# Performance work log

Measured on AMD Instinct MI355X. Metric: run time of the kernel, lower is better.

The kernel has to match this reference:

```python
import jax, jax.numpy as jnp
import numpy as np

B, N = 16, 300000          # batch, total anchors per image (all FPN levels concatenated)
PRE, POST = 2000, 1000     # num_pre_nms, num_post_nms
NMS_THR = 0.7
MIN_SIZE = 1e-3            # proposal_min_size
IMG_H, IMG_W = 800.0, 1333.0


def setup_inputs() -> dict:
    key = jax.random.key(0)
    k1, k2, k3, k4, k5, k6 = jax.random.split(key, 6)
    cls = jax.random.normal(k1, (B, N), dtype=jnp.float32)
    reg = jax.random.normal(k2, (B, N, 4), dtype=jnp.float32) * 0.1
    # anchors as valid (cx,cy,w,h)->(x1,y1,x2,y2) boxes inside the image
    cx = jax.random.uniform(k3, (B, N), dtype=jnp.float32, minval=0.0, maxval=IMG_W)
    cy = jax.random.uniform(k4, (B, N), dtype=jnp.float32, minval=0.0, maxval=IMG_H)
    w = jax.random.uniform(k5, (B, N), dtype=jnp.float32, minval=16.0, maxval=256.0)
    h = jax.random.uniform(k6, (B, N), dtype=jnp.float32, minval=16.0, maxval=256.0)
    anchors = jnp.stack([cx - 0.5 * w, cy - 0.5 * h, cx + 0.5 * w, cy + 0.5 * h], axis=-1)
    return {"cls": cls, "reg": reg, "anchors": anchors}


def _decode(anchor, reg):
    aw = anchor[:, 2] - anchor[:, 0]
    ah = anchor[:, 3] - anchor[:, 1]
    acx = anchor[:, 0] + 0.5 * aw
    acy = anchor[:, 1] + 0.5 * ah
    dx, dy, dw, dh = reg[:, 0], reg[:, 1], reg[:, 2], reg[:, 3]
    pcx = dx * aw + acx
    pcy = dy * ah + acy
    pw = jnp.exp(dw) * aw
    ph = jnp.exp(dh) * ah
    return jnp.stack([pcx - 0.5 * pw, pcy - 0.5 * ph, pcx + 0.5 * pw, pcy + 0.5 * ph], axis=-1)


def _iou_matrix(boxes):
    # boxes: [K,4] -> pairwise IoU [K,K]
    area = (boxes[:, 2] - boxes[:, 0]) * (boxes[:, 3] - boxes[:, 1])
    lt = jnp.maximum(boxes[:, None, :2], boxes[None, :, :2])
    rb = jnp.minimum(boxes[:, None, 2:], boxes[None, :, 2:])
    wh = jnp.clip(rb - lt, 0.0)
    inter = wh[..., 0] * wh[..., 1]
    union = area[:, None] + area[None, :] - inter
    return inter / jnp.maximum(union, 1e-8)


def _per_image(score, reg, anchor):
    # topk pre-NMS selection (lax.top_k returns score-descending order)
    top_s, idx = jax.lax.top_k(score, PRE)
    boxes = _decode(anchor[idx], reg[idx].reshape(-1, 4))
    # clip to image bounds
    bounds = jnp.array([IMG_W, IMG_H, IMG_W, IMG_H], dtype=boxes.dtype)
    boxes = jnp.clip(boxes, 0.0, bounds)
    # remove small boxes (mask instead of dynamic removal)
    w = boxes[:, 2] - boxes[:, 0]
    h = boxes[:, 3] - boxes[:, 1]
    valid = (w >= MIN_SIZE) & (h >= MIN_SIZE)
    s = jnp.where(valid, top_s, -jnp.inf)
    order = jnp.argsort(-s)  # score-descending, invalid last
    boxes = boxes[order]
    valid = valid[order]
    # greedy NMS: iterate highest-score-first, suppress later boxes with IoU > thr
    iou = _iou_matrix(boxes)
    rng = jnp.arange(PRE)
    def body(i, keep):
        sup = (iou[i] > NMS_THR) & keep[i]
        return keep & jnp.logical_not(sup & (rng > i))
    keep = jax.lax.fori_loop(0, PRE, body, valid)
    # gather kept boxes (score order preserved), pad with zeros past count
    sel = jnp.argsort(jnp.logical_not(keep), stable=True)[:POST]
    return boxes[sel] * keep[sel][:, None].astype(boxes.dtype)


def reference(cls, reg, anchors):
    # [B, POST, 4] proposals per image (zero-padded where fewer than POST kept)
    return jax.vmap(_per_image)(cls, reg, anchors)
```

## Files before the change

kernel.cpp:

```cpp
#include <hip/hip_runtime.h>

#define NB 16
#define NN 300000
#define PRE 2000
#define POST 1000

typedef unsigned long long ull;

static const size_t OFF_HIST1   = 0;
static const size_t OFF_CANDCNT = 65536;
static const size_t OFF_BINCNT  = 65792;
static const size_t OFF_B1      = 66048;
static const size_t OFF_NEED1   = 66304;
static const size_t OFF_NVALID  = 66560;
static const size_t OFF_BITMAP  = 66816;
static const size_t ZERO_BYTES  = 70912;
static const size_t OFF_CAND    = 70912;
static const size_t OFF_KEYS    = 201984;
static const size_t OFF_BOXTMP  = 464128;
static const size_t OFF_SORTED  = 988416;
static const size_t OFF_MASK    = 1500416;
static const size_t OFF_BINBUF  = OFF_MASK;

__device__ __forceinline__ unsigned f2u(float f){
  unsigned b = __float_as_uint(f);
  return (b & 0x80000000u) ? ~b : (b | 0x80000000u);
}

#define H1REP 8
#define H1STRIDE 1025
__global__ void k_hist1(const float* __restrict__ cls, unsigned* __restrict__ hist){
  __shared__ unsigned h[H1REP * H1STRIDE];
  int img = blockIdx.y;
  for (int i = threadIdx.x; i < H1REP * H1STRIDE; i += blockDim.x) h[i] = 0;
  __syncthreads();
  const float* p = cls + (size_t)img * NN;
  int stride = gridDim.x * blockDim.x;
  unsigned rep = (threadIdx.x & (H1REP - 1)) * H1STRIDE;
  for (int i = blockIdx.x * blockDim.x + threadIdx.x; i < NN; i += stride)
    atomicAdd(&h[rep + (f2u(p[i]) >> 22)], 1u);
  __syncthreads();
  unsigned* g = hist + img * 1024;
  for (int i = threadIdx.x; i < 1024; i += blockDim.x){
    unsigned v = 0;
    for (int r = 0; r < H1REP; r++) v += h[r * H1STRIDE + i];
    if (v) atomicAdd(&g[i], v);
  }
}

__global__ void k_scan(const unsigned* __restrict__ hist, int bins,
                       unsigned K0,
                       unsigned* __restrict__ outBin, unsigned* __restrict__ outNeed){
  int img = blockIdx.x;
  int t = threadIdx.x;
  const unsigned* hh = hist + img * bins;
  unsigned K = K0;
  int per = bins >> 8;
  unsigned s = 0;
  for (int q = 0; q < per; q++) s += hh[bins - 1 - (t * per + q)];
  __shared__ unsigned arr[256];
  arr[t] = s;
  __syncthreads();
  for (int off = 1; off < 256; off <<= 1){
    unsigned v = (t >= off) ? arr[t - off] : 0u;
    __syncthreads();
    arr[t] += v;
    __syncthreads();
  }
  unsigned incl = arr[t], excl = incl - s;
  if (excl < K && K <= incl){
    unsigned c = excl;
    for (int q = 0; q < per; q++){
      int b = bins - 1 - (t * per + q);
      unsigned cnt = hh[b];
      if (c + cnt >= K){ outBin[img] = (unsigned)b; outNeed[img] = K - c; break; }
      c += cnt;
    }
  }
}

__global__ void k_compactA(const float* __restrict__ cls, const unsigned* __restrict__ b1,
                           unsigned* __restrict__ cand, unsigned* __restrict__ candCnt,
                           ull* __restrict__ binbuf, unsigned* __restrict__ binCnt){
  __shared__ unsigned lc[1024];
  __shared__ ull lb[512];
  __shared__ unsigned lcn, lbn, baseC, baseB;
  int img = blockIdx.y;
  if (threadIdx.x == 0){ lcn = 0; lbn = 0; }
  __syncthreads();
  unsigned bb1 = b1[img];
  const float* p = cls + (size_t)img * NN;
  int stride = gridDim.x * blockDim.x;
  for (int i = blockIdx.x * blockDim.x + threadIdx.x; i < NN; i += stride){
    unsigned u = f2u(p[i]);
    unsigned top = u >> 22;
    if (top > bb1){
      unsigned pos = atomicAdd(&lcn, 1u);
      if (pos < 1024u) lc[pos] = (unsigned)i;
      else { unsigned g = atomicAdd(&candCnt[img], 1u); if (g < 2048u) cand[img * 2048 + g] = (unsigned)i; }
    } else if (top == bb1){
      ull e = ((ull)u << 32) | (unsigned)i;
      unsigned pos = atomicAdd(&lbn, 1u);
      if (pos < 512u) lb[pos] = e;
      else { unsigned g = atomicAdd(&binCnt[img], 1u); if (g < 8192u) binbuf[img * 8192 + g] = e; }
    }
  }
  __syncthreads();
  unsigned nc = lcn < 1024u ? lcn : 1024u;
  unsigned nb = lbn < 512u ? lbn : 512u;
  if (threadIdx.x == 0){
    if (nc) baseC = atomicAdd(&candCnt[img], nc);
    if (nb) baseB = atomicAdd(&binCnt[img], nb);
  }
  __syncthreads();
  for (unsigned t = threadIdx.x; t < nc; t += blockDim.x){
    unsigned g = baseC + t;
    if (g < 2048u) cand[img * 2048 + g] = lc[t];
  }
  for (unsigned t = threadIdx.x; t < nb; t += blockDim.x){
    unsigned g = baseB + t;
    if (g < 8192u) binbuf[img * 8192 + g] = lb[t];
  }
}

__global__ __launch_bounds__(256) void k_select(const float* __restrict__ cls,
                                                const float* __restrict__ reg,
                                                const float* __restrict__ anch,
                                                unsigned* __restrict__ cand,
                                                const unsigned* __restrict__ candCnt,
                                                const ull* __restrict__ binbuf,
                                                const unsigned* __restrict__ binCnt,
                                                const unsigned* __restrict__ need1,
                                                float* __restrict__ boxTmp,
                                                ull* __restrict__ keys,
                                                unsigned* __restrict__ nvalid){
  __shared__ unsigned hist[2048];
  __shared__ unsigned arr[256];
  __shared__ unsigned b2s, need2s, b3s, need3s;
  __shared__ unsigned tiePos[1024];
  __shared__ unsigned wcnt, tieCnt;
  int img = blockIdx.x, tid = threadIdx.x;
  unsigned bc = binCnt[img]; if (bc > 8192u) bc = 8192u;
  unsigned base = candCnt[img];
  unsigned need = need1[img];
  const ull* bb = binbuf + img * 8192;

  if (tid == 0){ wcnt = 0; tieCnt = 0; b2s = 0; need2s = 0; b3s = 0; need3s = 0; }
  for (int i = tid; i < 2048; i += 256) hist[i] = 0;
  __syncthreads();
  for (unsigned t = tid; t < bc; t += 256){
    unsigned u = (unsigned)(bb[t] >> 32);
    atomicAdd(&hist[(u >> 11) & 0x7FFu], 1u);
  }
  __syncthreads();
  {
    unsigned s = 0;
    for (int q = 0; q < 8; q++) s += hist[2047 - (tid * 8 + q)];
    arr[tid] = s; __syncthreads();
    for (int off = 1; off < 256; off <<= 1){
      unsigned v = (tid >= off) ? arr[tid - off] : 0u;
      __syncthreads(); arr[tid] += v; __syncthreads();
    }
    unsigned incl = arr[tid], excl = incl - s;
    if (excl < need && need <= incl){
      unsigned c = excl;
      for (int q = 0; q < 8; q++){
        int b = 2047 - (tid * 8 + q);
        unsigned cnt = hist[b];
        if (c + cnt >= need){ b2s = (unsigned)b; need2s = need - c; break; }
        c += cnt;
      }
    }
  }
  __syncthreads();
  unsigned b2 = b2s, need2 = need2s;
  for (int i = tid; i < 2048; i += 256) hist[i] = 0;
  __syncthreads();
  for (unsigned t = tid; t < bc; t += 256){
    unsigned u = (unsigned)(bb[t] >> 32);
    if (((u >> 11) & 0x7FFu) == b2) atomicAdd(&hist[u & 0x7FFu], 1u);
  }
  __syncthreads();
  {
    unsigned s = 0;
    for (int q = 0; q < 8; q++) s += hist[2047 - (tid * 8 + q)];
    arr[tid] = s; __syncthreads();
    for (int off = 1; off < 256; off <<= 1){
      unsigned v = (tid >= off) ? arr[tid - off] : 0u;
      __syncthreads(); arr[tid] += v; __syncthreads();
    }
    unsigned incl = arr[tid], excl = incl - s;
    if (excl < need2 && need2 <= incl){
      unsigned c = excl;
      for (int q = 0; q < 8; q++){
        int b = 2047 - (tid * 8 + q);
        unsigned cnt = hist[b];
        if (c + cnt >= need2){ b3s = (unsigned)b; need3s = need2 - c; break; }
        c += cnt;
      }
    }
  }
  __syncthreads();
  unsigned b3 = b3s, need3 = need3s;
  for (unsigned t = tid; t < bc; t += 256){
    ull e = bb[t];
    unsigned u = (unsigned)(e >> 32);
    unsigned mid = (u >> 11) & 0x7FFu, low = u & 0x7FFu;
    bool take = (mid > b2) || (mid == b2 && low > b3);
    bool tie  = (mid == b2) && (low == b3);
    if (take){
      unsigned p = atomicAdd(&wcnt, 1u);
      unsigned g = base + p;
      if (g < 2048u) cand[img * 2048 + g] = (unsigned)(e & 0xFFFFFFFFull);
    } else if (tie){
      unsigned p = atomicAdd(&tieCnt, 1u);
      if (p < 1024u) tiePos[p] = t;
    }
  }
  __syncthreads();
  unsigned above = wcnt;
  unsigned ec = tieCnt; if (ec > 1024u) ec = 1024u;
  for (unsigned t = tid; t < ec; t += 256){
    unsigned idx = (unsigned)(bb[tiePos[t]] & 0xFFFFFFFFull);
    unsigned r = 0;
    for (unsigned s = 0; s < ec; s++){
      unsigned idx2 = (unsigned)(bb[tiePos[s]] & 0xFFFFFFFFull);
      r += (idx2 < idx) ? 1u : 0u;
    }
    if (r < need3){
      unsigned g = base + above + r;
      if (g < 2048u) cand[img * 2048 + g] = idx;
    }
  }
  __syncthreads();
  for (int slot = tid; slot < 2048; slot += 256){
    ull key = 0ull;
    float4 box = make_float4(0.f, 0.f, 0.f, 0.f);
    bool counted = false;
    if (slot < PRE){
      unsigned i = cand[img * 2048 + slot];
      if (i < NN){
        size_t gi = (size_t)img * NN + i;
        float4 a = ((const float4*)anch)[gi];
        float4 r = ((const float4*)reg)[gi];
        float sc = cls[gi];
        float aw = a.z - a.x, ah = a.w - a.y;
        float acx = a.x + 0.5f * aw, acy = a.y + 0.5f * ah;
        float pcx = r.x * aw + acx, pcy = r.y * ah + acy;
        float pw = expf(r.z) * aw, ph = expf(r.w) * ah;
        float x1 = pcx - 0.5f * pw, y1 = pcy - 0.5f * ph;
        float x2 = pcx + 0.5f * pw, y2 = pcy + 0.5f * ph;
        x1 = fminf(fmaxf(x1, 0.f), 1333.f); x2 = fminf(fmaxf(x2, 0.f), 1333.f);
        y1 = fminf(fmaxf(y1, 0.f), 800.f);  y2 = fminf(fmaxf(y2, 0.f), 800.f);
        bool valid = ((x2 - x1) >= 0.001f) && ((y2 - y1) >= 0.001f);
        unsigned up = valid ? f2u(sc) : 0u;
        key = ((ull)up << 32) | (ull)(0xFFFFFFFFu - i);
        box = make_float4(x1, y1, x2, y2);
        counted = valid;
      }
    }
    keys[img * 2048 + slot] = key;
    ((float4*)boxTmp)[img * 2048 + slot] = box;
    ull bal = __ballot(counted);
    if ((tid & 63) == 0 && bal)
      atomicAdd(&nvalid[img], (unsigned)__popcll(bal));
  }
}

__global__ __launch_bounds__(256) void k_rank(const ull* __restrict__ keys,
                                              const float* __restrict__ boxTmp,
                                              float* __restrict__ sorted){
  __shared__ ull lk[2048];
  int img = blockIdx.y;
  int e = blockIdx.x * 256 + threadIdx.x;
  for (int t = threadIdx.x; t < 2048; t += 256) lk[t] = keys[img * 2048 + t];
  __syncthreads();
  ull me = lk[e];
  unsigned rank = 0;
  #pragma unroll 8
  for (int j = 0; j < 2048; j++) rank += (lk[j] > me) ? 1u : 0u;
  if (rank < PRE)
    ((float4*)sorted)[img * PRE + rank] = ((const float4*)boxTmp)[img * 2048 + e];
}

__global__ __launch_bounds__(512) void k_mask(const float* __restrict__ sorted,
                                              const unsigned* __restrict__ nvalid,
                                              ull* __restrict__ mask, ull* __restrict__ bitmap){
  __shared__ float4 bx[PRE];
  __shared__ float  ar[PRE];
  int img = blockIdx.y, tid = threadIdx.x;
  int jmin = blockIdx.x * 16;
  for (int i = jmin + tid; i < PRE; i += 512){
    float4 b = ((const float4*)sorted)[img * PRE + i];
    bx[i] = b;
    ar[i] = (b.z - b.x) * (b.w - b.y);
  }
  __syncthreads();
  int unit = tid >> 5;
  int w = tid & 31;
  int lane = tid & 63;
  int nv = (int)nvalid[img];
  int qhi = ((PRE - 1 - w) >> 5) + 1;
  int rowF = jmin + unit;
  #pragma unroll
  for (int rr = 0; rr < 2; rr++){
    int row = (rr == 0) ? rowF : (PRE - 1 - rowF);
    float4 bi = bx[row];
    float ai = ar[row];
    int qlo = (row >= w) ? (((row - w) >> 5) + 1) : 0;
    ull m = 0;
    for (int q = qlo; q < qhi; q++){
      int j = (q << 5) + w;
      float4 bj = bx[j];
      float xx1 = fmaxf(bi.x, bj.x), yy1 = fmaxf(bi.y, bj.y);
      float xx2 = fminf(bi.z, bj.z), yy2 = fminf(bi.w, bj.w);
      float ww = fmaxf(xx2 - xx1, 0.f), hh = fmaxf(yy2 - yy1, 0.f);
      float inter = ww * hh;
      float uni = ai + ar[j] - inter;
      if (inter / fmaxf(uni, 1e-8f) > 0.7f) m |= (1ull << q);
    }
    mask[((size_t)(img * PRE + row)) * 32 + w] = m;
    ull nz = __ballot(m != 0ull);
    if (lane == 0 || lane == 32){
      ull half = (lane == 0) ? (nz & 0xFFFFFFFFull) : (nz >> 32);
      if (half && row < nv)
        atomicOr(&bitmap[img * 32 + (row >> 6)], 1ull << (row & 63));
    }
  }
}

#define CHR 48
__global__ __launch_bounds__(256) void k_nms(const ull* __restrict__ mask,
                                             const ull* __restrict__ bitmap,
                                             const unsigned* __restrict__ nvalid,
                                             const float* __restrict__ sorted,
                                             float* __restrict__ out){
  __shared__ unsigned rowsLds[2048];
  __shared__ unsigned cntw[32];
  __shared__ unsigned wbaseS[32];
  __shared__ int mcountS, mpS;
  __shared__ ull cacheD[2][CHR * 32];
  __shared__ ull keepP[32];
  __shared__ ull keepLin[32];
  __shared__ unsigned cntArr[32], preArr[32];
  int img = blockIdx.x, tid = threadIdx.x;
  int lane = tid & 63, wave = tid >> 6;

  if (tid < 32) cntw[tid] = (unsigned)__popcll(bitmap[img * 32 + tid]);
  __syncthreads();
  if (tid == 0){
    unsigned s = 0;
    for (int w0 = 0; w0 < 32; w0++){ wbaseS[w0] = s; s += cntw[w0]; }
    mcountS = (int)s;
    mpS = ((int)s + CHR - 1) / CHR * CHR;
  }
  __syncthreads();
  int m = mcountS, mp = mpS;
  if (tid < 32){
    ull bits = bitmap[img * 32 + tid];
    unsigned pos = wbaseS[tid];
    int base_i = tid * 64;
    while (bits){
      int b = __ffsll((long long)bits) - 1;
      rowsLds[pos++] = (unsigned)(base_i + b);
      bits &= bits - 1;
    }
  }
  for (int t = m + tid; t < mp; t += 256) rowsLds[t] = PRE - 1;
  __syncthreads();

  int nch = mp / CHR;
  ull remv = 0;
  const ull* mg = mask + (size_t)img * PRE * 32;

  if (nch > 0 && tid >= 64){
    int s = tid - 64;
    ull v[8];
    #pragma unroll
    for (int k = 0; k < 8; k++){
      int t = k * 192 + s;
      unsigned rr = rowsLds[t >> 5];
      v[k] = mg[(size_t)rr * 32 + (t & 31)];
    }
    #pragma unroll
    for (int k = 0; k < 8; k++) cacheD[0][k * 192 + s] = v[k];
  }
  __syncthreads();

  for (int c = 0; c < nch; c++){
    int cb = c & 1;
    if (tid >= 64){
      if (c + 1 < nch){
        int q0n = (c + 1) * CHR;
        int s = tid - 64;
        ull v[8];
        #pragma unroll
        for (int k = 0; k < 8; k++){
          int t = k * 192 + s;
          unsigned rr = rowsLds[q0n + (t >> 5)];
          v[k] = mg[(size_t)rr * 32 + (t & 31)];
        }
        #pragma unroll
        for (int k = 0; k < 8; k++) cacheD[cb ^ 1][k * 192 + s] = v[k];
      }
    } else {
      const ull* cbuf = cacheD[cb];
      const int q0 = c * CHR;
      ull cur[8]; unsigned ci[8];
      #pragma unroll
      for (int k = 0; k < 8; k++){
        ci[k] = rowsLds[q0 + k];
        cur[k] = cbuf[(k << 5) | (lane & 31)];
      }
      #pragma unroll
      for (int g = 0; g < 6; g++){
        ull nxt[8]; unsigned ni[8];
        if (g < 5){
          #pragma unroll
          for (int k = 0; k < 8; k++){
            int lq = (g + 1) * 8 + k;
            ni[k] = rowsLds[q0 + lq];
            nxt[k] = cbuf[(lq << 5) | (lane & 31)];
          }
        }
        #pragma unroll
        for (int k = 0; k < 8; k++){
          unsigned i = ci[k];
          unsigned bit = ((unsigned)(remv >> (i >> 5))) & 1u;
          int sup = (lane == (int)(i & 31)) && bit;
          if (!__any(sup)) remv |= cur[k];
        }
        if (g < 5){
          #pragma unroll
          for (int k = 0; k < 8; k++){ cur[k] = nxt[k]; ci[k] = ni[k]; }
        }
      }
    }
    __syncthreads();
  }

  int nv = (int)nvalid[img];
  if (wave == 0 && lane < 32){
    int cnt2 = (nv > lane) ? (((nv - 1 - lane) >> 5) + 1) : 0;
    ull vm = (cnt2 >= 64) ? ~0ull : ((1ull << cnt2) - 1ull);
    keepP[lane] = (~remv) & vm;
  }
  __syncthreads();
  if (tid < 32){
    ull lin = 0;
    for (int kk = 0; kk < 64; kk++)
      lin |= ((keepP[kk & 31] >> (2 * tid + (kk >> 5))) & 1ull) << kk;
    keepLin[tid] = lin;
    cntArr[tid] = (unsigned)__popcll(lin);
  }
  __syncthreads();
  if (tid < 32){
    unsigned pre = 0;
    for (int w0 = 0; w0 < tid; w0++) pre += cntArr[w0];
    preArr[tid] = pre;
  }
  __syncthreads();
  int totK = (int)(preArr[31] + cntArr[31]);
  for (int i = tid; i < PRE; i += 256){
    int w0 = i >> 6, b = i & 63;
    ull kw = keepLin[w0];
    if ((kw >> b) & 1ull){
      unsigned rank = preArr[w0] + (unsigned)__popcll(kw & ((1ull << b) - 1ull));
      if (rank < POST)
        ((float4*)out)[img * POST + rank] = ((const float4*)sorted)[img * PRE + i];
    }
  }
  for (int r = totK + tid; r < POST; r += 256)
    ((float4*)out)[img * POST + r] = make_float4(0.f, 0.f, 0.f, 0.f);
}

extern "C" void kernel_launch(void* const* d_in, const int* in_sizes, int n_in,
                              void* d_out, int out_size, void* d_ws, size_t ws_size,
                              hipStream_t stream){
  const float* cls  = (const float*)d_in[0];
  const float* reg  = (const float*)d_in[1];
  const float* anch = (const float*)d_in[2];
  float* out = (float*)d_out;
  char* ws = (char*)d_ws;

  unsigned* hist1   = (unsigned*)(ws + OFF_HIST1);
  unsigned* candCnt = (unsigned*)(ws + OFF_CANDCNT);
  unsigned* binCnt  = (unsigned*)(ws + OFF_BINCNT);
  unsigned* b1      = (unsigned*)(ws + OFF_B1);
  unsigned* need1   = (unsigned*)(ws + OFF_NEED1);
  unsigned* nvalid  = (unsigned*)(ws + OFF_NVALID);
  ull*      bitmap  = (ull*)     (ws + OFF_BITMAP);
  unsigned* cand    = (unsigned*)(ws + OFF_CAND);
  ull*      keys    = (ull*)     (ws + OFF_KEYS);
  float*    boxTmp  = (float*)   (ws + OFF_BOXTMP);
  float*    sorted  = (float*)   (ws + OFF_SORTED);
  ull*      maskG   = (ull*)     (ws + OFF_MASK);
  ull*      binbuf  = (ull*)     (ws + OFF_BINBUF);

  hipMemsetAsync(ws, 0, ZERO_BYTES, stream);

  k_hist1   <<<dim3(64, NB), 256, 0, stream>>>(cls, hist1);
  k_scan    <<<NB, 256, 0, stream>>>(hist1, 1024, 2000u, b1, need1);
  k_compactA<<<dim3(64, NB), 256, 0, stream>>>(cls, b1, cand, candCnt, binbuf, binCnt);
  k_select  <<<NB, 256, 0, stream>>>(cls, reg, anch, cand, candCnt, binbuf, binCnt,
                                     need1, boxTmp, keys, nvalid);
  k_rank    <<<dim3(8, NB), 256, 0, stream>>>(keys, boxTmp, sorted);
  k_mask    <<<dim3(63, NB), 512, 0, stream>>>(sorted, nvalid, maskG, bitmap);
  k_nms     <<<NB, 256, 0, stream>>>(maskG, bitmap, nvalid, sorted, out);
}
```

Measured before the change: 302.5 us.

## Fuse score histogram with speculative high-score stash; drop scan and compaction kernels

The histogram kernel now also appends (key, index) pairs for every score whose top 10 bits are at or above a fixed bin into a per-image stash. The threshold scan and the second full compaction pass over the scores are removed; k_select computes the first threshold itself and filters candidates from the stash. If the chosen bin falls below the stash threshold, or the stash overflows, it falls back to scanning all scores. This removes one full read of the score array and two kernel launches. In exchange it adds stash writes in the histogram pass and longer single-block loops in k_select, and it adds an unroll hint to the IoU mask loop.

```diff
diff --git a/kernel.cpp b/kernel.cpp
--- a/kernel.cpp
+++ b/kernel.cpp
@@ -8,10 +8,7 @@
 typedef unsigned long long ull;
 
 static const size_t OFF_HIST1   = 0;
-static const size_t OFF_CANDCNT = 65536;
-static const size_t OFF_BINCNT  = 65792;
-static const size_t OFF_B1      = 66048;
-static const size_t OFF_NEED1   = 66304;
+static const size_t OFF_STASHC  = 65536;
 static const size_t OFF_NVALID  = 66560;
 static const size_t OFF_BITMAP  = 66816;
 static const size_t ZERO_BYTES  = 70912;
@@ -20,7 +17,10 @@
 static const size_t OFF_BOXTMP  = 464128;
 static const size_t OFF_SORTED  = 988416;
 static const size_t OFF_MASK    = 1500416;
-static const size_t OFF_BINBUF  = OFF_MASK;
+static const size_t OFF_STASH   = OFF_MASK;
+
+#define BSTAT 767u
+#define STCAP 32768u
 
 __device__ __forceinline__ unsigned f2u(float f){
   unsigned b = __float_as_uint(f);
@@ -29,17 +29,37 @@
 
 #define H1REP 8
 #define H1STRIDE 1025
-__global__ void k_hist1(const float* __restrict__ cls, unsigned* __restrict__ hist){
+__global__ void k_histstash(const float* __restrict__ cls, unsigned* __restrict__ hist,
+                            ull* __restrict__ stash, unsigned* __restrict__ stashCnt){
   __shared__ unsigned h[H1REP * H1STRIDE];
+  __shared__ ull lb[512];
+  __shared__ unsigned lbn, baseB;
   int img = blockIdx.y;
   for (int i = threadIdx.x; i < H1REP * H1STRIDE; i += blockDim.x) h[i] = 0;
+  if (threadIdx.x == 0) lbn = 0;
   __syncthreads();
   const float* p = cls + (size_t)img * NN;
   int stride = gridDim.x * blockDim.x;
   unsigned rep = (threadIdx.x & (H1REP - 1)) * H1STRIDE;
-  for (int i = blockIdx.x * blockDim.x + threadIdx.x; i < NN; i += stride)
-    atomicAdd(&h[rep + (f2u(p[i]) >> 22)], 1u);
-  __syncthreads();
+  ull* st = stash + (size_t)img * STCAP;
+  for (int i = blockIdx.x * blockDim.x + threadIdx.x; i < NN; i += stride){
+    unsigned u = f2u(p[i]);
+    atomicAdd(&h[rep + (u >> 22)], 1u);
+    if ((u >> 22) >= BSTAT){
+      ull e = ((ull)u << 32) | (unsigned)i;
+      unsigned pos = atomicAdd(&lbn, 1u);
+      if (pos < 512u) lb[pos] = e;
+      else { unsigned g = atomicAdd(&stashCnt[img], 1u); if (g < STCAP) st[g] = e; }
+    }
+  }
+  __syncthreads();
+  unsigned nb = lbn < 512u ? lbn : 512u;
+  if (threadIdx.x == 0 && nb) baseB = atomicAdd(&stashCnt[img], nb);
+  __syncthreads();
+  for (unsigned t = threadIdx.x; t < nb; t += blockDim.x){
+    unsigned g = baseB + t;
+    if (g < STCAP) st[g] = lb[t];
+  }
   unsigned* g = hist + img * 1024;
   for (int i = threadIdx.x; i < 1024; i += blockDim.x){
     unsigned v = 0;
@@ -48,109 +68,64 @@
   }
 }
 
-__global__ void k_scan(const unsigned* __restrict__ hist, int bins,
-                       unsigned K0,
-                       unsigned* __restrict__ outBin, unsigned* __restrict__ outNeed){
-  int img = blockIdx.x;
-  int t = threadIdx.x;
-  const unsigned* hh = hist + img * bins;
-  unsigned K = K0;
-  int per = bins >> 8;
-  unsigned s = 0;
-  for (int q = 0; q < per; q++) s += hh[bins - 1 - (t * per + q)];
-  __shared__ unsigned arr[256];
-  arr[t] = s;
-  __syncthreads();
-  for (int off = 1; off < 256; off <<= 1){
-    unsigned v = (t >= off) ? arr[t - off] : 0u;
-    __syncthreads();
-    arr[t] += v;
-    __syncthreads();
-  }
-  unsigned incl = arr[t], excl = incl - s;
-  if (excl < K && K <= incl){
-    unsigned c = excl;
-    for (int q = 0; q < per; q++){
-      int b = bins - 1 - (t * per + q);
-      unsigned cnt = hh[b];
-      if (c + cnt >= K){ outBin[img] = (unsigned)b; outNeed[img] = K - c; break; }
-      c += cnt;
-    }
-  }
-}
-
-__global__ void k_compactA(const float* __restrict__ cls, const unsigned* __restrict__ b1,
-                           unsigned* __restrict__ cand, unsigned* __restrict__ candCnt,
-                           ull* __restrict__ binbuf, unsigned* __restrict__ binCnt){
-  __shared__ unsigned lc[1024];
-  __shared__ ull lb[512];
-  __shared__ unsigned lcn, lbn, baseC, baseB;
-  int img = blockIdx.y;
-  if (threadIdx.x == 0){ lcn = 0; lbn = 0; }
-  __syncthreads();
-  unsigned bb1 = b1[img];
-  const float* p = cls + (size_t)img * NN;
-  int stride = gridDim.x * blockDim.x;
-  for (int i = blockIdx.x * blockDim.x + threadIdx.x; i < NN; i += stride){
-    unsigned u = f2u(p[i]);
-    unsigned top = u >> 22;
-    if (top > bb1){
-      unsigned pos = atomicAdd(&lcn, 1u);
-      if (pos < 1024u) lc[pos] = (unsigned)i;
-      else { unsigned g = atomicAdd(&candCnt[img], 1u); if (g < 2048u) cand[img * 2048 + g] = (unsigned)i; }
-    } else if (top == bb1){
-      ull e = ((ull)u << 32) | (unsigned)i;
-      unsigned pos = atomicAdd(&lbn, 1u);
-      if (pos < 512u) lb[pos] = e;
-      else { unsigned g = atomicAdd(&binCnt[img], 1u); if (g < 8192u) binbuf[img * 8192 + g] = e; }
-    }
-  }
-  __syncthreads();
-  unsigned nc = lcn < 1024u ? lcn : 1024u;
-  unsigned nb = lbn < 512u ? lbn : 512u;
-  if (threadIdx.x == 0){
-    if (nc) baseC = atomicAdd(&candCnt[img], nc);
-    if (nb) baseB = atomicAdd(&binCnt[img], nb);
-  }
-  __syncthreads();
-  for (unsigned t = threadIdx.x; t < nc; t += blockDim.x){
-    unsigned g = baseC + t;
-    if (g < 2048u) cand[img * 2048 + g] = lc[t];
-  }
-  for (unsigned t = threadIdx.x; t < nb; t += blockDim.x){
-    unsigned g = baseB + t;
-    if (g < 8192u) binbuf[img * 8192 + g] = lb[t];
-  }
-}
-
 __global__ __launch_bounds__(256) void k_select(const float* __restrict__ cls,
                                                 const float* __restrict__ reg,
                                                 const float* __restrict__ anch,
+                                                const unsigned* __restrict__ hist1,
                                                 unsigned* __restrict__ cand,
-                                                const unsigned* __restrict__ candCnt,
-                                                const ull* __restrict__ binbuf,
-                                                const unsigned* __restrict__ binCnt,
-                                                const unsigned* __restrict__ need1,
+                                                const ull* __restrict__ stash,
+                                                const unsigned* __restrict__ stashCnt,
                                                 float* __restrict__ boxTmp,
                                                 ull* __restrict__ keys,
                                                 unsigned* __restrict__ nvalid){
   __shared__ unsigned hist[2048];
   __shared__ unsigned arr[256];
-  __shared__ unsigned b2s, need2s, b3s, need3s;
+  __shared__ unsigned b1s, need1s, b2s, need2s, b3s, need3s;
   __shared__ unsigned tiePos[1024];
   __shared__ unsigned wcnt, tieCnt;
   int img = blockIdx.x, tid = threadIdx.x;
-  unsigned bc = binCnt[img]; if (bc > 8192u) bc = 8192u;
-  unsigned base = candCnt[img];
-  unsigned need = need1[img];
-  const ull* bb = binbuf + img * 8192;
-
-  if (tid == 0){ wcnt = 0; tieCnt = 0; b2s = 0; need2s = 0; b3s = 0; need3s = 0; }
+  const float* pcls = cls + (size_t)img * NN;
+  const ull* st = stash + (size_t)img * STCAP;
+
+  if (tid == 0){ wcnt = 0; tieCnt = 0; b1s = 0; need1s = 0; b2s = 0; need2s = 0; b3s = 0; need3s = 0; }
+  {
+    const unsigned* hh = hist1 + img * 1024;
+    unsigned s = 0;
+    for (int q = 0; q < 4; q++) s += hh[1023 - (tid * 4 + q)];
+    arr[tid] = s; __syncthreads();
+    for (int off = 1; off < 256; off <<= 1){
+      unsigned v = (tid >= off) ? arr[tid - off] : 0u;
+      __syncthreads(); arr[tid] += v; __syncthreads();
+    }
+    unsigned incl = arr[tid], excl = incl - s;
+    if (excl < 2000u && 2000u <= incl){
+      unsigned c = excl;
+      for (int q = 0; q < 4; q++){
+        int b = 1023 - (tid * 4 + q);
+        unsigned cnt = hh[b];
+        if (c + cnt >= 2000u){ b1s = (unsigned)b; need1s = 2000u - c; break; }
+        c += cnt;
+      }
+    }
+  }
   for (int i = tid; i < 2048; i += 256) hist[i] = 0;
   __syncthreads();
-  for (unsigned t = tid; t < bc; t += 256){
-    unsigned u = (unsigned)(bb[t] >> 32);
-    atomicAdd(&hist[(u >> 11) & 0x7FFu], 1u);
+  unsigned b1 = b1s, need = need1s;
+  unsigned sc = stashCnt[img];
+  bool fb = (b1 < BSTAT) || (sc > STCAP);
+  unsigned Nit = fb ? (unsigned)NN : sc;
+
+  for (unsigned t = tid; t < Nit; t += 256){
+    unsigned u, idx;
+    if (fb){ u = f2u(pcls[t]); idx = t; }
+    else { ull e = st[t]; u = (unsigned)(e >> 32); idx = (unsigned)(e & 0xFFFFFFFFull); }
+    unsigned top = u >> 22;
+    if (top > b1){
+      unsigned p = atomicAdd(&wcnt, 1u);
+      if (p < 2048u) cand[img * 2048 + p] = idx;
+    } else if (top == b1){
+      atomicAdd(&hist[(u >> 11) & 0x7FFu], 1u);
+    }
   }
   __syncthreads();
   {
@@ -176,9 +151,11 @@
   unsigned b2 = b2s, need2 = need2s;
   for (int i = tid; i < 2048; i += 256) hist[i] = 0;
   __syncthreads();
-  for (unsigned t = tid; t < bc; t += 256){
-    unsigned u = (unsigned)(bb[t] >> 32);
-    if (((u >> 11) & 0x7FFu) == b2) atomicAdd(&hist[u & 0x7FFu], 1u);
+  for (unsigned t = tid; t < Nit; t += 256){
+    unsigned u;
+    if (fb) u = f2u(pcls[t]);
+    else u = (unsigned)(st[t] >> 32);
+    if ((u >> 22) == b1 && ((u >> 11) & 0x7FFu) == b2) atomicAdd(&hist[u & 0x7FFu], 1u);
   }
   __syncthreads();
   {
@@ -202,33 +179,34 @@
   }
   __syncthreads();
   unsigned b3 = b3s, need3 = need3s;
-  for (unsigned t = tid; t < bc; t += 256){
-    ull e = bb[t];
-    unsigned u = (unsigned)(e >> 32);
+  for (unsigned t = tid; t < Nit; t += 256){
+    unsigned u, idx;
+    if (fb){ u = f2u(pcls[t]); idx = t; }
+    else { ull e = st[t]; u = (unsigned)(e >> 32); idx = (unsigned)(e & 0xFFFFFFFFull); }
+    if ((u >> 22) != b1) continue;
     unsigned mid = (u >> 11) & 0x7FFu, low = u & 0x7FFu;
     bool take = (mid > b2) || (mid == b2 && low > b3);
     bool tie  = (mid == b2) && (low == b3);
     if (take){
       unsigned p = atomicAdd(&wcnt, 1u);
-      unsigned g = base + p;
-      if (g < 2048u) cand[img * 2048 + g] = (unsigned)(e & 0xFFFFFFFFull);
+      if (p < 2048u) cand[img * 2048 + p] = idx;
     } else if (tie){
       unsigned p = atomicAdd(&tieCnt, 1u);
       if (p < 1024u) tiePos[p] = t;
     }
   }
   __syncthreads();
-  unsigned above = wcnt;
+  unsigned tbase = wcnt;
   unsigned ec = tieCnt; if (ec > 1024u) ec = 1024u;
   for (unsigned t = tid; t < ec; t += 256){
-    unsigned idx = (unsigned)(bb[tiePos[t]] & 0xFFFFFFFFull);
+    unsigned idx = fb ? tiePos[t] : (unsigned)(st[tiePos[t]] & 0xFFFFFFFFull);
     unsigned r = 0;
     for (unsigned s = 0; s < ec; s++){
-      unsigned idx2 = (unsigned)(bb[tiePos[s]] & 0xFFFFFFFFull);
+      unsigned idx2 = fb ? tiePos[s] : (unsigned)(st[tiePos[s]] & 0xFFFFFFFFull);
       r += (idx2 < idx) ? 1u : 0u;
     }
     if (r < need3){
-      unsigned g = base + above + r;
+      unsigned g = tbase + r;
       if (g < 2048u) cand[img * 2048 + g] = idx;
     }
   }
@@ -243,7 +221,7 @@
         size_t gi = (size_t)img * NN + i;
         float4 a = ((const float4*)anch)[gi];
         float4 r = ((const float4*)reg)[gi];
-        float sc = cls[gi];
+        float sc2 = cls[gi];
         float aw = a.z - a.x, ah = a.w - a.y;
         float acx = a.x + 0.5f * aw, acy = a.y + 0.5f * ah;
         float pcx = r.x * aw + acx, pcy = r.y * ah + acy;
@@ -253,7 +231,7 @@
         x1 = fminf(fmaxf(x1, 0.f), 1333.f); x2 = fminf(fmaxf(x2, 0.f), 1333.f);
         y1 = fminf(fmaxf(y1, 0.f), 800.f);  y2 = fminf(fmaxf(y2, 0.f), 800.f);
         bool valid = ((x2 - x1) >= 0.001f) && ((y2 - y1) >= 0.001f);
-        unsigned up = valid ? f2u(sc) : 0u;
+        unsigned up = valid ? f2u(sc2) : 0u;
         key = ((ull)up << 32) | (ull)(0xFFFFFFFFu - i);
         box = make_float4(x1, y1, x2, y2);
         counted = valid;
@@ -309,6 +287,7 @@
     float ai = ar[row];
     int qlo = (row >= w) ? (((row - w) >> 5) + 1) : 0;
     ull m = 0;
+    #pragma unroll 2
     for (int q = qlo; q < qhi; q++){
       int j = (q << 5) + w;
       float4 bj = bx[j];
@@ -483,28 +462,23 @@
   float* out = (float*)d_out;
   char* ws = (char*)d_ws;
 
-  unsigned* hist1   = (unsigned*)(ws + OFF_HIST1);
-  unsigned* candCnt = (unsigned*)(ws + OFF_CANDCNT);
-  unsigned* binCnt  = (unsigned*)(ws + OFF_BINCNT);
-  unsigned* b1      = (unsigned*)(ws + OFF_B1);
-  unsigned* need1   = (unsigned*)(ws + OFF_NEED1);
-  unsigned* nvalid  = (unsigned*)(ws + OFF_NVALID);
-  ull*      bitmap  = (ull*)     (ws + OFF_BITMAP);
-  unsigned* cand    = (unsigned*)(ws + OFF_CAND);
-  ull*      keys    = (ull*)     (ws + OFF_KEYS);
-  float*    boxTmp  = (float*)   (ws + OFF_BOXTMP);
-  float*    sorted  = (float*)   (ws + OFF_SORTED);
-  ull*      maskG   = (ull*)     (ws + OFF_MASK);
-  ull*      binbuf  = (ull*)     (ws + OFF_BINBUF);
+  unsigned* hist1    = (unsigned*)(ws + OFF_HIST1);
+  unsigned* stashCnt = (unsigned*)(ws + OFF_STASHC);
+  unsigned* nvalid   = (unsigned*)(ws + OFF_NVALID);
+  ull*      bitmap   = (ull*)     (ws + OFF_BITMAP);
+  unsigned* cand     = (unsigned*)(ws + OFF_CAND);
+  ull*      keys     = (ull*)     (ws + OFF_KEYS);
+  float*    boxTmp   = (float*)   (ws + OFF_BOXTMP);
+  float*    sorted   = (float*)   (ws + OFF_SORTED);
+  ull*      maskG    = (ull*)     (ws + OFF_MASK);
+  ull*      stash    = (ull*)     (ws + OFF_STASH);
 
   hipMemsetAsync(ws, 0, ZERO_BYTES, stream);
 
-  k_hist1   <<<dim3(64, NB), 256, 0, stream>>>(cls, hist1);
-  k_scan    <<<NB, 256, 0, stream>>>(hist1, 1024, 2000u, b1, need1);
-  k_compactA<<<dim3(64, NB), 256, 0, stream>>>(cls, b1, cand, candCnt, binbuf, binCnt);
-  k_select  <<<NB, 256, 0, stream>>>(cls, reg, anch, cand, candCnt, binbuf, binCnt,
-                                     need1, boxTmp, keys, nvalid);
-  k_rank    <<<dim3(8, NB), 256, 0, stream>>>(keys, boxTmp, sorted);
-  k_mask    <<<dim3(63, NB), 512, 0, stream>>>(sorted, nvalid, maskG, bitmap);
-  k_nms     <<<NB, 256, 0, stream>>>(maskG, bitmap, nvalid, sorted, out);
-}
+  k_histstash<<<dim3(64, NB), 256, 0, stream>>>(cls, hist1, stash, stashCnt);
+  k_select   <<<NB, 256, 0, stream>>>(cls, reg, anch, hist1, cand, stash, stashCnt,
+                                      boxTmp, keys, nvalid);
+  k_rank     <<<dim3(8, NB), 256, 0, stream>>>(keys, boxTmp, sorted);
+  k_mask     <<<dim3(63, NB), 512, 0, stream>>>(sorted, nvalid, maskG, bitmap);
+  k_nms      <<<NB, 256, 0, stream>>>(maskG, bitmap, nvalid, sorted, out);
+}
```

After: 343.9 us. +13.7%, slower.

## Stash high-score candidates during histogram pass to skip second full scan

Applied to the files above, without the earlier changes.

The histogram kernel now also writes every element whose top bits are at or above a fixed threshold bin into a per-image stash buffer. The compaction kernel then scans only this small stash instead of re-reading all 300k scores, with a fallback to the full scan when the selection bin falls below the threshold or the stash overflows. This removes the second full pass over the score array and lets compaction run with fewer blocks. In exchange the histogram pass does extra atomics and global writes, and it needs more workspace. The IoU mask loop also gets an unroll pragma.

```diff
diff --git a/kernel.cpp b/kernel.cpp
--- a/kernel.cpp
+++ b/kernel.cpp
@@ -8,19 +8,24 @@
 typedef unsigned long long ull;
 
 static const size_t OFF_HIST1   = 0;
-static const size_t OFF_CANDCNT = 65536;
-static const size_t OFF_BINCNT  = 65792;
-static const size_t OFF_B1      = 66048;
-static const size_t OFF_NEED1   = 66304;
-static const size_t OFF_NVALID  = 66560;
-static const size_t OFF_BITMAP  = 66816;
-static const size_t ZERO_BYTES  = 70912;
-static const size_t OFF_CAND    = 70912;
-static const size_t OFF_KEYS    = 201984;
-static const size_t OFF_BOXTMP  = 464128;
-static const size_t OFF_SORTED  = 988416;
-static const size_t OFF_MASK    = 1500416;
-static const size_t OFF_BINBUF  = OFF_MASK;
+static const size_t OFF_STASHC  = 65536;
+static const size_t OFF_CANDCNT = 65792;
+static const size_t OFF_BINCNT  = 66048;
+static const size_t OFF_B1      = 66304;
+static const size_t OFF_NEED1   = 66560;
+static const size_t OFF_NVALID  = 66816;
+static const size_t OFF_BITMAP  = 67072;
+static const size_t ZERO_BYTES  = 71168;
+static const size_t OFF_CAND    = 71168;
+static const size_t OFF_KEYS    = 202240;
+static const size_t OFF_BOXTMP  = 464384;
+static const size_t OFF_SORTED  = 988672;
+static const size_t OFF_MASK    = 1500672;
+static const size_t OFF_STASH   = OFF_MASK;
+static const size_t OFF_BINBUF  = OFF_MASK + 4194304;
+
+#define BSTAT 767u
+#define STCAP 32768u
 
 __device__ __forceinline__ unsigned f2u(float f){
   unsigned b = __float_as_uint(f);
@@ -29,17 +34,37 @@
 
 #define H1REP 8
 #define H1STRIDE 1025
-__global__ void k_hist1(const float* __restrict__ cls, unsigned* __restrict__ hist){
+__global__ void k_histstash(const float* __restrict__ cls, unsigned* __restrict__ hist,
+                            ull* __restrict__ stash, unsigned* __restrict__ stashCnt){
   __shared__ unsigned h[H1REP * H1STRIDE];
+  __shared__ ull lb[512];
+  __shared__ unsigned lbn, baseB;
   int img = blockIdx.y;
   for (int i = threadIdx.x; i < H1REP * H1STRIDE; i += blockDim.x) h[i] = 0;
+  if (threadIdx.x == 0) lbn = 0;
   __syncthreads();
   const float* p = cls + (size_t)img * NN;
   int stride = gridDim.x * blockDim.x;
   unsigned rep = (threadIdx.x & (H1REP - 1)) * H1STRIDE;
-  for (int i = blockIdx.x * blockDim.x + threadIdx.x; i < NN; i += stride)
-    atomicAdd(&h[rep + (f2u(p[i]) >> 22)], 1u);
-  __syncthreads();
+  ull* st = stash + (size_t)img * STCAP;
+  for (int i = blockIdx.x * blockDim.x + threadIdx.x; i < NN; i += stride){
+    unsigned u = f2u(p[i]);
+    atomicAdd(&h[rep + (u >> 22)], 1u);
+    if ((u >> 22) >= BSTAT){
+      ull e = ((ull)u << 32) | (unsigned)i;
+      unsigned pos = atomicAdd(&lbn, 1u);
+      if (pos < 512u) lb[pos] = e;
+      else { unsigned g = atomicAdd(&stashCnt[img], 1u); if (g < STCAP) st[g] = e; }
+    }
+  }
+  __syncthreads();
+  unsigned nb = lbn < 512u ? lbn : 512u;
+  if (threadIdx.x == 0 && nb) baseB = atomicAdd(&stashCnt[img], nb);
+  __syncthreads();
+  for (unsigned t = threadIdx.x; t < nb; t += blockDim.x){
+    unsigned g = baseB + t;
+    if (g < STCAP) st[g] = lb[t];
+  }
   unsigned* g = hist + img * 1024;
   for (int i = threadIdx.x; i < 1024; i += blockDim.x){
     unsigned v = 0;
@@ -48,16 +73,14 @@
   }
 }
 
-__global__ void k_scan(const unsigned* __restrict__ hist, int bins,
-                       unsigned K0,
+__global__ void k_scan(const unsigned* __restrict__ hist, unsigned K0,
                        unsigned* __restrict__ outBin, unsigned* __restrict__ outNeed){
   int img = blockIdx.x;
   int t = threadIdx.x;
-  const unsigned* hh = hist + img * bins;
+  const unsigned* hh = hist + img * 1024;
   unsigned K = K0;
-  int per = bins >> 8;
   unsigned s = 0;
-  for (int q = 0; q < per; q++) s += hh[bins - 1 - (t * per + q)];
+  for (int q = 0; q < 4; q++) s += hh[1023 - (t * 4 + q)];
   __shared__ unsigned arr[256];
   arr[t] = s;
   __syncthreads();
@@ -70,8 +93,8 @@
   unsigned incl = arr[t], excl = incl - s;
   if (excl < K && K <= incl){
     unsigned c = excl;
-    for (int q = 0; q < per; q++){
-      int b = bins - 1 - (t * per + q);
+    for (int q = 0; q < 4; q++){
+      int b = 1023 - (t * 4 + q);
       unsigned cnt = hh[b];
       if (c + cnt >= K){ outBin[img] = (unsigned)b; outNeed[img] = K - c; break; }
       c += cnt;
@@ -79,7 +102,8 @@
   }
 }
 
-__global__ void k_compactA(const float* __restrict__ cls, const unsigned* __restrict__ b1,
+__global__ void k_compactS(const float* __restrict__ cls, const ull* __restrict__ stash,
+                           const unsigned* __restrict__ stashCnt, const unsigned* __restrict__ b1,
                            unsigned* __restrict__ cand, unsigned* __restrict__ candCnt,
                            ull* __restrict__ binbuf, unsigned* __restrict__ binCnt){
   __shared__ unsigned lc[1024];
@@ -89,20 +113,39 @@
   if (threadIdx.x == 0){ lcn = 0; lbn = 0; }
   __syncthreads();
   unsigned bb1 = b1[img];
-  const float* p = cls + (size_t)img * NN;
+  unsigned sc = stashCnt[img];
+  bool fb = (bb1 < BSTAT) || (sc > STCAP);
   int stride = gridDim.x * blockDim.x;
-  for (int i = blockIdx.x * blockDim.x + threadIdx.x; i < NN; i += stride){
-    unsigned u = f2u(p[i]);
-    unsigned top = u >> 22;
-    if (top > bb1){
-      unsigned pos = atomicAdd(&lcn, 1u);
-      if (pos < 1024u) lc[pos] = (unsigned)i;
-      else { unsigned g = atomicAdd(&candCnt[img], 1u); if (g < 2048u) cand[img * 2048 + g] = (unsigned)i; }
-    } else if (top == bb1){
-      ull e = ((ull)u << 32) | (unsigned)i;
-      unsigned pos = atomicAdd(&lbn, 1u);
-      if (pos < 512u) lb[pos] = e;
-      else { unsigned g = atomicAdd(&binCnt[img], 1u); if (g < 8192u) binbuf[img * 8192 + g] = e; }
+  if (!fb){
+    const ull* st = stash + (size_t)img * STCAP;
+    for (unsigned t = blockIdx.x * blockDim.x + threadIdx.x; t < sc; t += (unsigned)stride){
+      ull e = st[t];
+      unsigned top = (unsigned)(e >> 54);
+      if (top > bb1){
+        unsigned pos = atomicAdd(&lcn, 1u);
+        if (pos < 1024u) lc[pos] = (unsigned)(e & 0xFFFFFFFFull);
+        else { unsigned g = atomicAdd(&candCnt[img], 1u); if (g < 2048u) cand[img * 2048 + g] = (unsigned)(e & 0xFFFFFFFFull); }
+      } else if (top == bb1){
+        unsigned pos = atomicAdd(&lbn, 1u);
+        if (pos < 512u) lb[pos] = e;
+        else { unsigned g = atomicAdd(&binCnt[img], 1u); if (g < 8192u) binbuf[img * 8192 + g] = e; }
+      }
+    }
+  } else {
+    const float* p = cls + (size_t)img * NN;
+    for (int i = blockIdx.x * blockDim.x + threadIdx.x; i < NN; i += stride){
+      unsigned u = f2u(p[i]);
+      unsigned top = u >> 22;
+      if (top > bb1){
+        unsigned pos = atomicAdd(&lcn, 1u);
+        if (pos < 1024u) lc[pos] = (unsigned)i;
+        else { unsigned g = atomicAdd(&candCnt[img], 1u); if (g < 2048u) cand[img * 2048 + g] = (unsigned)i; }
+      } else if (top == bb1){
+        ull e = ((ull)u << 32) | (unsigned)i;
+        unsigned pos = atomicAdd(&lbn, 1u);
+        if (pos < 512u) lb[pos] = e;
+        else { unsigned g = atomicAdd(&binCnt[img], 1u); if (g < 8192u) binbuf[img * 8192 + g] = e; }
+      }
     }
   }
   __syncthreads();
@@ -243,7 +286,7 @@
         size_t gi = (size_t)img * NN + i;
         float4 a = ((const float4*)anch)[gi];
         float4 r = ((const float4*)reg)[gi];
-        float sc = cls[gi];
+        float sc2 = cls[gi];
         float aw = a.z - a.x, ah = a.w - a.y;
         float acx = a.x + 0.5f * aw, acy = a.y + 0.5f * ah;
         float pcx = r.x * aw + acx, pcy = r.y * ah + acy;
@@ -253,7 +296,7 @@
         x1 = fminf(fmaxf(x1, 0.f), 1333.f); x2 = fminf(fmaxf(x2, 0.f), 1333.f);
         y1 = fminf(fmaxf(y1, 0.f), 800.f);  y2 = fminf(fmaxf(y2, 0.f), 800.f);
         bool valid = ((x2 - x1) >= 0.001f) && ((y2 - y1) >= 0.001f);
-        unsigned up = valid ? f2u(sc) : 0u;
+        unsigned up = valid ? f2u(sc2) : 0u;
         key = ((ull)up << 32) | (ull)(0xFFFFFFFFu - i);
         box = make_float4(x1, y1, x2, y2);
         counted = valid;
@@ -309,6 +352,7 @@
     float ai = ar[row];
     int qlo = (row >= w) ? (((row - w) >> 5) + 1) : 0;
     ull m = 0;
+    #pragma unroll 2
     for (int q = qlo; q < qhi; q++){
       int j = (q << 5) + w;
       float4 bj = bx[j];
@@ -483,28 +527,30 @@
   float* out = (float*)d_out;
   char* ws = (char*)d_ws;
 
-  unsigned* hist1   = (unsigned*)(ws + OFF_HIST1);
-  unsigned* candCnt = (unsigned*)(ws + OFF_CANDCNT);
-  unsigned* binCnt  = (unsigned*)(ws + OFF_BINCNT);
-  unsigned* b1      = (unsigned*)(ws + OFF_B1);
-  unsigned* need1   = (unsigned*)(ws + OFF_NEED1);
-  unsigned* nvalid  = (unsigned*)(ws + OFF_NVALID);
-  ull*      bitmap  = (ull*)     (ws + OFF_BITMAP);
-  unsigned* cand    = (unsigned*)(ws + OFF_CAND);
-  ull*      keys    = (ull*)     (ws + OFF_KEYS);
-  float*    boxTmp  = (float*)   (ws + OFF_BOXTMP);
-  float*    sorted  = (float*)   (ws + OFF_SORTED);
-  ull*      maskG   = (ull*)     (ws + OFF_MASK);
-  ull*      binbuf  = (ull*)     (ws + OFF_BINBUF);
+  unsigned* hist1    = (unsigned*)(ws + OFF_HIST1);
+  unsigned* stashCnt = (unsigned*)(ws + OFF_STASHC);
+  unsigned* candCnt  = (unsigned*)(ws + OFF_CANDCNT);
+  unsigned* binCnt   = (unsigned*)(ws + OFF_BINCNT);
+  unsigned* b1       = (unsigned*)(ws + OFF_B1);
+  unsigned* need1    = (unsigned*)(ws + OFF_NEED1);
+  unsigned* nvalid   = (unsigned*)(ws + OFF_NVALID);
+  ull*      bitmap   = (ull*)     (ws + OFF_BITMAP);
+  unsigned* cand     = (unsigned*)(ws + OFF_CAND);
+  ull*      keys     = (ull*)     (ws + OFF_KEYS);
+  float*    boxTmp   = (float*)   (ws + OFF_BOXTMP);
+  float*    sorted   = (float*)   (ws + OFF_SORTED);
+  ull*      maskG    = (ull*)     (ws + OFF_MASK);
+  ull*      stash    = (ull*)     (ws + OFF_STASH);
+  ull*      binbuf   = (ull*)     (ws + OFF_BINBUF);
 
   hipMemsetAsync(ws, 0, ZERO_BYTES, stream);
 
-  k_hist1   <<<dim3(64, NB), 256, 0, stream>>>(cls, hist1);
-  k_scan    <<<NB, 256, 0, stream>>>(hist1, 1024, 2000u, b1, need1);
-  k_compactA<<<dim3(64, NB), 256, 0, stream>>>(cls, b1, cand, candCnt, binbuf, binCnt);
-  k_select  <<<NB, 256, 0, stream>>>(cls, reg, anch, cand, candCnt, binbuf, binCnt,
-                                     need1, boxTmp, keys, nvalid);
-  k_rank    <<<dim3(8, NB), 256, 0, stream>>>(keys, boxTmp, sorted);
-  k_mask    <<<dim3(63, NB), 512, 0, stream>>>(sorted, nvalid, maskG, bitmap);
-  k_nms     <<<NB, 256, 0, stream>>>(maskG, bitmap, nvalid, sorted, out);
-}
+  k_histstash<<<dim3(64, NB), 256, 0, stream>>>(cls, hist1, stash, stashCnt);
+  k_scan     <<<NB, 256, 0, stream>>>(hist1, 2000u, b1, need1);
+  k_compactS <<<dim3(8, NB), 256, 0, stream>>>(cls, stash, stashCnt, b1, cand, candCnt, binbuf, binCnt);
+  k_select   <<<NB, 256, 0, stream>>>(cls, reg, anch, cand, candCnt, binbuf, binCnt,
+                                      need1, boxTmp, keys, nvalid);
+  k_rank     <<<dim3(8, NB), 256, 0, stream>>>(keys, boxTmp, sorted);
+  k_mask     <<<dim3(63, NB), 512, 0, stream>>>(sorted, nvalid, maskG, bitmap);
+  k_nms      <<<NB, 256, 0, stream>>>(maskG, bitmap, nvalid, sorted, out);
+}
```

After: 320.8 us. 1.06x slower.
